# Optimization experiments

Hardware: AMD Instinct MI355X
Metric: run time of the kernel (lower is better)

## Reference

```python
import jax, jax.numpy as jnp
import numpy as np

N = 40000      # nodes
E = 640000     # edges (before self-loops)
F_IN = 32      # num_node_features
H = 8          # n_heads
C = 16         # hidden_channels
G = 1000       # graphs in batch
M = 256        # MLP_neurons
NEG_SLOPE = 0.2


def setup_inputs() -> dict:
    key = jax.random.key(0)
    ks = jax.random.split(key, 24)
    d = {}
    d["x"] = jax.random.normal(ks[0], (N, F_IN), jnp.float32)
    d["edge_index"] = jax.random.randint(ks[1], (2, E), 0, N, dtype=jnp.int32)
    d["batch"] = jnp.sort(jax.random.randint(ks[2], (N,), 0, G, dtype=jnp.int32))
    dims = [F_IN, H * C, H * C]
    k = 3
    for i in range(3):
        fin = dims[i]
        s = 1.0 / np.sqrt(fin)
        d[f"W{i}"] = jax.random.normal(ks[k], (fin, H * C), jnp.float32) * s; k += 1
        d[f"b{i}"] = jnp.zeros((H * C,), jnp.float32)
        d[f"as{i}"] = jax.random.normal(ks[k], (H, C), jnp.float32) * (1.0 / np.sqrt(C)); k += 1
        d[f"ad{i}"] = jax.random.normal(ks[k], (H, C), jnp.float32) * (1.0 / np.sqrt(C)); k += 1
    d["fW0"] = jax.random.normal(ks[k], (H * C, M), jnp.float32) * (1.0 / np.sqrt(H * C)); k += 1
    d["fb0"] = jnp.zeros((M,), jnp.float32)
    d["fW1"] = jax.random.normal(ks[k], (M, M), jnp.float32) * (1.0 / np.sqrt(M)); k += 1
    d["fb1"] = jnp.zeros((M,), jnp.float32)
    d["oW"] = jax.random.normal(ks[k], (M, 2), jnp.float32) * (1.0 / np.sqrt(M)); k += 1
    d["ob"] = jnp.zeros((2,), jnp.float32)
    return d


def _gat_layer(x, W, b, a_src, a_dst, src, dst):
    # x: [N, Fin] -> h: [N, H, C]
    h = (x @ W).reshape(N, H, C)
    al_src = jnp.einsum('nhc,hc->nh', h, a_src)   # [N, H]
    al_dst = jnp.einsum('nhc,hc->nh', h, a_dst)   # [N, H]
    # edge-wise attention logits (gather), LeakyReLU
    e = jax.nn.leaky_relu(al_src[src] + al_dst[dst], NEG_SLOPE)  # [E', H]
    # softmax over incoming edges of each dst node
    emax = jax.ops.segment_max(e, dst, num_segments=N)           # [N, H]
    ex = jnp.exp(e - emax[dst])
    denom = jax.ops.segment_sum(ex, dst, num_segments=N)         # [N, H]
    alpha = ex / denom[dst]
    # weighted scatter-aggregation of source features
    out = jax.ops.segment_sum(alpha[:, :, None] * h[src], dst, num_segments=N)  # [N, H, C]
    return out.reshape(N, H * C) + b


def reference(x, edge_index, batch, W0, b0, as0, ad0, W1, b1, as1, ad1,
              W2, b2, as2, ad2, fW0, fb0, fW1, fb1, oW, ob):
    # PyG GATConv adds self-loops by default
    loops = jnp.arange(N, dtype=edge_index.dtype)
    src = jnp.concatenate([edge_index[0], loops])
    dst = jnp.concatenate([edge_index[1], loops])
    h = x
    for (W, b, a_s, a_d) in ((W0, b0, as0, ad0), (W1, b1, as1, ad1), (W2, b2, as2, ad2)):
        h = jax.nn.relu(_gat_layer(h, W, b, a_s, a_d, src, dst))
    # global mean pool per graph
    sums = jax.ops.segment_sum(h, batch, num_segments=G)                    # [G, H*C]
    cnts = jax.ops.segment_sum(jnp.ones((N,), h.dtype), batch, num_segments=G)
    g = sums / jnp.maximum(cnts, 1.0)[:, None]
    # MLP head (dropout is identity in eval mode)
    g = jax.nn.relu(g @ fW0 + fb0)
    g = jax.nn.relu(g @ fW1 + fb1)
    return g @ oW + ob
```

## Files before the change

### kernel.cpp

```cpp
#include <hip/hip_runtime.h>
#include <hip/hip_fp16.h>
#include <math.h>

#define NN 40000
#define EE 640000
#define EP 680000
#define FIN0 32
#define HC 128
#define GG 1000
#define MM 256
#define SCAN_BLOCKS ((NN + 255) / 256)


__global__ void hist_kernel(const int* __restrict__ ei, int* __restrict__ deg,
                            int* __restrict__ rank) {
    int idx = blockIdx.x * 256 + threadIdx.x;
    if (idx >= EP) return;
    int d = (idx < EE) ? ei[EE + idx] : (idx - EE);
    rank[idx] = atomicAdd(&deg[d], 1);
}

__global__ __launch_bounds__(256) void scan_partial(const int* __restrict__ deg,
                                                    int* __restrict__ part) {
    int b = blockIdx.x, t = threadIdx.x;
    int i = b * 256 + t;
    int v = (i < NN) ? deg[i] : 0;
#pragma unroll
    for (int d = 1; d < 64; d <<= 1) v += __shfl_xor(v, d);
    __shared__ int ws[4];
    if ((t & 63) == 0) ws[t >> 6] = v;
    __syncthreads();
    if (t == 0) part[b] = ws[0] + ws[1] + ws[2] + ws[3];
}

__global__ __launch_bounds__(256) void scan_final(const int* __restrict__ deg,
                                                  const int* __restrict__ part,
                                                  int* __restrict__ offs) {
    int b = blockIdx.x, t = threadIdx.x;
    __shared__ int sbase;
    if (t < 64) {
        int s = 0;
        for (int l = t; l < b; l += 64) s += part[l];
#pragma unroll
        for (int d = 1; d < 64; d <<= 1) s += __shfl_xor(s, d);
        if (t == 0) sbase = s;
    }
    int i = b * 256 + t;
    int v = (i < NN) ? deg[i] : 0;
    __shared__ int tmp[256];
    tmp[t] = v;
    __syncthreads();
    for (int st = 1; st < 256; st <<= 1) {
        int add = (t >= st) ? tmp[t - st] : 0;
        __syncthreads();
        tmp[t] += add;
        __syncthreads();
    }
    int excl = tmp[t] - v + sbase;
    if (i < NN) offs[i] = excl;
    if (i == NN - 1) offs[NN] = excl + v;
}

__global__ void scatter_kernel(const int* __restrict__ ei, const int* __restrict__ offs,
                               const int* __restrict__ rank, int* __restrict__ esrc) {
    int idx = blockIdx.x * 256 + threadIdx.x;
    if (idx >= EP) return;
    int s, d;
    if (idx < EE) { s = ei[idx]; d = ei[EE + idx]; } else { s = idx - EE; d = s; }
    esrc[offs[d] + rank[idx]] = s;
}


template <int FIN>
__global__ __launch_bounds__(256) void proj_kernel(const float* __restrict__ X,
                                                   const float* __restrict__ W,
                                                   const float* __restrict__ a_src,
                                                   const float* __restrict__ a_dst,
                                                   __half* __restrict__ H2,
                                                   float* __restrict__ als,
                                                   float* __restrict__ ald) {
    constexpr int KT = 32;
    static_assert(FIN % KT == 0, "FIN % KT");
    __shared__ float xs[KT][68];
    __shared__ float ws[KT][128];
    int t = threadIdx.x;
    int node0 = blockIdx.x * 64;
    int nt = t & 15;
    int ct = t >> 4;
    float acc[4][8];
#pragma unroll
    for (int i = 0; i < 4; i++)
#pragma unroll
        for (int j = 0; j < 8; j++) acc[i][j] = 0.f;

    for (int kk = 0; kk < FIN; kk += KT) {
#pragma unroll
        for (int r = 0; r < (64 * KT) / 256; r++) {
            int idx = r * 256 + t;
            int n = idx / KT, k = idx % KT;
            xs[k][n] = X[(node0 + n) * FIN + kk + k];
        }
#pragma unroll
        for (int r = 0; r < (KT * 128) / 256; r++) {
            int idx = r * 256 + t;
            int k = idx >> 7, c = idx & 127;
            ws[k][c] = W[(kk + k) * 128 + c];
        }
        __syncthreads();
#pragma unroll
        for (int k = 0; k < KT; k++) {
            const float4 xv = *(const float4*)(&xs[k][4 * nt]);
            const float4 wa = *(const float4*)(&ws[k][8 * ct]);
            const float4 wb = *(const float4*)(&ws[k][8 * ct + 4]);
            float xr[4] = {xv.x, xv.y, xv.z, xv.w};
            float wr[8] = {wa.x, wa.y, wa.z, wa.w, wb.x, wb.y, wb.z, wb.w};
#pragma unroll
            for (int i = 0; i < 4; i++)
#pragma unroll
                for (int j = 0; j < 8; j++) acc[i][j] = fmaf(xr[i], wr[j], acc[i][j]);
        }
        __syncthreads();
    }
#pragma unroll
    for (int i = 0; i < 4; i++) {
        int n = node0 + 4 * nt + i;
        __half2 p0 = __floats2half2_rn(acc[i][0], acc[i][1]);
        __half2 p1 = __floats2half2_rn(acc[i][2], acc[i][3]);
        __half2 p2 = __floats2half2_rn(acc[i][4], acc[i][5]);
        __half2 p3 = __floats2half2_rn(acc[i][6], acc[i][7]);
        uint4 pk;
        pk.x = *(unsigned*)&p0; pk.y = *(unsigned*)&p1;
        pk.z = *(unsigned*)&p2; pk.w = *(unsigned*)&p3;
        *(uint4*)(&H2[(size_t)n * HC + 8 * ct]) = pk;
    }
    float sa[4] = {0.f, 0.f, 0.f, 0.f}, da[4] = {0.f, 0.f, 0.f, 0.f};
#pragma unroll
    for (int j = 0; j < 8; j++) {
        float av = a_src[ct * 8 + j];
        float dv = a_dst[ct * 8 + j];
#pragma unroll
        for (int i = 0; i < 4; i++) {
            sa[i] = fmaf(acc[i][j], av, sa[i]);
            da[i] = fmaf(acc[i][j], dv, da[i]);
        }
    }
#pragma unroll
    for (int i = 0; i < 4; i++) {
        sa[i] += __shfl_xor(sa[i], 16);
        da[i] += __shfl_xor(da[i], 16);
    }
    if ((ct & 1) == 0) {
        int head = ct >> 1;
#pragma unroll
        for (int i = 0; i < 4; i++) {
            int n = node0 + 4 * nt + i;
            als[n * 8 + head] = sa[i];
            ald[n * 8 + head] = da[i];
        }
    }
}


__global__ __launch_bounds__(256) void agg_kernel(const __half* __restrict__ H2,
                                                  const float* __restrict__ als,
                                                  const float* __restrict__ ald,
                                                  const int* __restrict__ offs,
                                                  const int* __restrict__ esrc,
                                                  const float* __restrict__ bias,
                                                  float* __restrict__ OUT) {
    int t = threadIdx.x;
    int n = blockIdx.x * 4 + (t >> 6);
    int t6 = t & 63;
    int c8 = t6 & 15;
    int slot = (t6 >> 4) & 3;
    int hd = c8 >> 1;
    int beg = offs[n], end = offs[n + 1];
    float ad = ald[n * 8 + hd];
    float acc[8] = {0.f, 0.f, 0.f, 0.f, 0.f, 0.f, 0.f, 0.f};
    float denom = 0.f;
    const float4* H4 = (const float4*)H2;

    int p = beg + slot;
    int s_cur = 0; float al_cur = 0.f;
    if (p < end) {
        s_cur = esrc[p];
        al_cur = als[s_cur * 8 + hd];
    }
#pragma unroll 2
    while (p < end) {
        int pn = p + 4;
        int s_nxt = 0;
        if (pn < end) s_nxt = esrc[pn];
        float x = al_cur + ad;
        x = (x > 0.f) ? x : 0.2f * x;
        float w = __expf(x);
        float4 r = H4[(size_t)s_cur * 16 + c8];
        float al_nxt = 0.f;
        if (pn < end) al_nxt = als[s_nxt * 8 + hd];
        __half2 h0 = *(__half2*)&r.x;
        __half2 h1 = *(__half2*)&r.y;
        __half2 h2 = *(__half2*)&r.z;
        __half2 h3 = *(__half2*)&r.w;
        float2 f0 = __half22float2(h0);
        float2 f1 = __half22float2(h1);
        float2 f2 = __half22float2(h2);
        float2 f3 = __half22float2(h3);
        acc[0] = fmaf(w, f0.x, acc[0]); acc[1] = fmaf(w, f0.y, acc[1]);
        acc[2] = fmaf(w, f1.x, acc[2]); acc[3] = fmaf(w, f1.y, acc[3]);
        acc[4] = fmaf(w, f2.x, acc[4]); acc[5] = fmaf(w, f2.y, acc[5]);
        acc[6] = fmaf(w, f3.x, acc[6]); acc[7] = fmaf(w, f3.y, acc[7]);
        denom += w;
        s_cur = s_nxt; al_cur = al_nxt;
        p = pn;
    }
#pragma unroll
    for (int j = 0; j < 8; j++) {
        acc[j] += __shfl_xor(acc[j], 16);
        acc[j] += __shfl_xor(acc[j], 32);
    }
    denom += __shfl_xor(denom, 16);
    denom += __shfl_xor(denom, 32);
    if (slot == 0 && t6 < 16) {
        float inv = 1.0f / denom;
        const float4 ba = ((const float4*)bias)[2 * c8];
        const float4 bb = ((const float4*)bias)[2 * c8 + 1];
        float4 o0, o1;
        o0.x = fmaxf(fmaf(acc[0], inv, ba.x), 0.f);
        o0.y = fmaxf(fmaf(acc[1], inv, ba.y), 0.f);
        o0.z = fmaxf(fmaf(acc[2], inv, ba.z), 0.f);
        o0.w = fmaxf(fmaf(acc[3], inv, ba.w), 0.f);
        o1.x = fmaxf(fmaf(acc[4], inv, bb.x), 0.f);
        o1.y = fmaxf(fmaf(acc[5], inv, bb.y), 0.f);
        o1.z = fmaxf(fmaf(acc[6], inv, bb.z), 0.f);
        o1.w = fmaxf(fmaf(acc[7], inv, bb.w), 0.f);
        ((float4*)OUT)[(size_t)n * 32 + 2 * c8]     = o0;
        ((float4*)OUT)[(size_t)n * 32 + 2 * c8 + 1] = o1;
    }
}


__global__ __launch_bounds__(256) void mlp_fused(const float* __restrict__ B,
                                                 const int* __restrict__ batch,
                                                 const float* __restrict__ fW0,
                                                 const float* __restrict__ fb0,
                                                 const float* __restrict__ fW1,
                                                 const float* __restrict__ fb1,
                                                 const float* __restrict__ oW,
                                                 const float* __restrict__ ob,
                                                 float* __restrict__ out) {
    __shared__ int lo[3];
    __shared__ float rows[2][128];
    __shared__ float g1s[2][256];
    __shared__ float g2s[2][256];
    int t = threadIdx.x;
    int g0 = blockIdx.x * 2;
    if (t < 3) {
        int target = g0 + t;
        int a = 0, b = NN;
        while (a < b) { int mid = (a + b) >> 1; if (batch[mid] < target) a = mid + 1; else b = mid; }
        lo[t] = a;
    }
    __syncthreads();
    {
        int j = t >> 7, c = t & 127;
        int s0 = lo[j], s1 = lo[j + 1];
        float s = 0.f;
        float p0 = 0.f, p1 = 0.f, p2 = 0.f, p3 = 0.f;
        int n = s0;
        for (; n + 3 < s1; n += 4) {
            p0 += B[(size_t)n * 128 + c];
            p1 += B[(size_t)(n + 1) * 128 + c];
            p2 += B[(size_t)(n + 2) * 128 + c];
            p3 += B[(size_t)(n + 3) * 128 + c];
        }
        for (; n < s1; n++) s += B[(size_t)n * 128 + c];
        s += (p0 + p1) + (p2 + p3);
        rows[j][c] = s / fmaxf((float)(s1 - s0), 1.0f);
    }
    __syncthreads();
    float a0 = 0.f, a1 = 0.f;
#pragma unroll 8
    for (int k = 0; k < 128; k++) {
        float w = fW0[k * 256 + t];
        a0 = fmaf(rows[0][k], w, a0);
        a1 = fmaf(rows[1][k], w, a1);
    }
    float b0v = fb0[t];
    g1s[0][t] = fmaxf(a0 + b0v, 0.f);
    g1s[1][t] = fmaxf(a1 + b0v, 0.f);
    __syncthreads();
    a0 = 0.f; a1 = 0.f;
#pragma unroll 8
    for (int k = 0; k < 256; k++) {
        float w = fW1[k * 256 + t];
        a0 = fmaf(g1s[0][k], w, a0);
        a1 = fmaf(g1s[1][k], w, a1);
    }
    float b1v = fb1[t];
    g2s[0][t] = fmaxf(a0 + b1v, 0.f);
    g2s[1][t] = fmaxf(a1 + b1v, 0.f);
    __syncthreads();
    if (t < 64) {
        int jj = t >> 5, l = t & 31;
        float p0 = 0.f, p1 = 0.f;
#pragma unroll
        for (int k = l; k < 256; k += 32) {
            float v = g2s[jj][k];
            p0 = fmaf(v, oW[k * 2 + 0], p0);
            p1 = fmaf(v, oW[k * 2 + 1], p1);
        }
#pragma unroll
        for (int d = 1; d < 32; d <<= 1) {
            p0 += __shfl_xor(p0, d);
            p1 += __shfl_xor(p1, d);
        }
        if (l == 0) {
            out[(g0 + jj) * 2 + 0] = p0 + ob[0];
            out[(g0 + jj) * 2 + 1] = p1 + ob[1];
        }
    }
}


extern "C" void kernel_launch(void* const* d_in, const int* in_sizes, int n_in,
                              void* d_out, int out_size, void* d_ws, size_t ws_size,
                              hipStream_t stream) {
    const float* x    = (const float*)d_in[0];
    const int* ei     = (const int*)d_in[1];
    const int* batch  = (const int*)d_in[2];
    const float* W[3]   = {(const float*)d_in[3], (const float*)d_in[7],  (const float*)d_in[11]};
    const float* bs[3]  = {(const float*)d_in[4], (const float*)d_in[8],  (const float*)d_in[12]};
    const float* asr[3] = {(const float*)d_in[5], (const float*)d_in[9],  (const float*)d_in[13]};
    const float* adt[3] = {(const float*)d_in[6], (const float*)d_in[10], (const float*)d_in[14]};
    const float* fW0 = (const float*)d_in[15];
    const float* fb0 = (const float*)d_in[16];
    const float* fW1 = (const float*)d_in[17];
    const float* fb1 = (const float*)d_in[18];
    const float* oW  = (const float*)d_in[19];
    const float* ob  = (const float*)d_in[20];
    float* out = (float*)d_out;

    char* base = (char*)d_ws;
    size_t off = 0;
    auto alloc = [&](size_t bytes) -> void* {
        void* p = base + off;
        off += (bytes + 255) & ~(size_t)255;
        return p;
    };
    int* deg    = (int*)alloc((size_t)NN * 4);
    int* offs   = (int*)alloc((size_t)(NN + 1) * 4);
    int* part   = (int*)alloc((size_t)SCAN_BLOCKS * 4);
    int* rank   = (int*)alloc((size_t)EP * 4);
    int* esrc   = (int*)alloc((size_t)EP * 4);
    __half* H2  = (__half*)alloc((size_t)NN * HC * 2);
    float* B    = (float*)alloc((size_t)NN * HC * 4);
    float* als  = (float*)alloc((size_t)NN * 8 * 4);
    float* ald  = (float*)alloc((size_t)NN * 8 * 4);

    hipMemsetAsync(deg, 0, (size_t)NN * 4, stream);

    hist_kernel<<<(EP + 255) / 256, 256, 0, stream>>>(ei, deg, rank);
    scan_partial<<<SCAN_BLOCKS, 256, 0, stream>>>(deg, part);
    scan_final<<<SCAN_BLOCKS, 256, 0, stream>>>(deg, part, offs);
    scatter_kernel<<<(EP + 255) / 256, 256, 0, stream>>>(ei, offs, rank, esrc);

    const float* cur = x;
    for (int l = 0; l < 3; l++) {
        if (l == 0) proj_kernel<FIN0><<<NN / 64, 256, 0, stream>>>(cur, W[l], asr[l], adt[l], H2, als, ald);
        else        proj_kernel<HC><<<NN / 64, 256, 0, stream>>>(cur, W[l], asr[l], adt[l], H2, als, ald);
        agg_kernel<<<NN / 4, 256, 0, stream>>>(H2, als, ald, offs, esrc, bs[l], B);
        cur = B;
    }
    mlp_fused<<<GG / 2, 256, 0, stream>>>(B, batch, fW0, fb0, fW1, fb1, oW, ob, out);
}
```

Measured before the change: 319.6 us.

## Enlarge projection tile to 128 nodes, vectorize loads, merge scan kernels

The projection GEMM now computes 128 nodes per block, with an 8x8 register tile per thread instead of 4x8, and loads X and W with float4 accesses. Bounds guards handle the partial last tile. The two-pass prefix scan becomes a single kernel in which each block directly sums all preceding degrees, removing one launch at the cost of redundant reads. The larger register tile raises register pressure, and with only 313 blocks occupancy may drop.

```diff
diff --git a/kernel.cpp b/kernel.cpp
--- a/kernel.cpp
+++ b/kernel.cpp
@@ -10,6 +10,7 @@
 #define GG 1000
 #define MM 256
 #define SCAN_BLOCKS ((NN + 255) / 256)
+#define PROJ_BLOCKS ((NN + 127) / 128)
 
 
 __global__ void hist_kernel(const int* __restrict__ ei, int* __restrict__ deg,
@@ -20,31 +21,19 @@
     rank[idx] = atomicAdd(&deg[d], 1);
 }
 
-__global__ __launch_bounds__(256) void scan_partial(const int* __restrict__ deg,
-                                                    int* __restrict__ part) {
+
+__global__ __launch_bounds__(256) void scan_kernel(const int* __restrict__ deg,
+                                                   int* __restrict__ offs) {
     int b = blockIdx.x, t = threadIdx.x;
-    int i = b * 256 + t;
-    int v = (i < NN) ? deg[i] : 0;
-#pragma unroll
-    for (int d = 1; d < 64; d <<= 1) v += __shfl_xor(v, d);
-    __shared__ int ws[4];
-    if ((t & 63) == 0) ws[t >> 6] = v;
-    __syncthreads();
-    if (t == 0) part[b] = ws[0] + ws[1] + ws[2] + ws[3];
-}
-
-__global__ __launch_bounds__(256) void scan_final(const int* __restrict__ deg,
-                                                  const int* __restrict__ part,
-                                                  int* __restrict__ offs) {
-    int b = blockIdx.x, t = threadIdx.x;
-    __shared__ int sbase;
-    if (t < 64) {
-        int s = 0;
-        for (int l = t; l < b; l += 64) s += part[l];
-#pragma unroll
-        for (int d = 1; d < 64; d <<= 1) s += __shfl_xor(s, d);
-        if (t == 0) sbase = s;
-    }
+    int s = 0;
+    for (int i = t; i < b * 256; i += 256) s += deg[i];
+#pragma unroll
+    for (int d = 1; d < 64; d <<= 1) s += __shfl_xor(s, d);
+    __shared__ int wsum[4];
+    if ((t & 63) == 0) wsum[t >> 6] = s;
+    __syncthreads();
+    int base = wsum[0] + wsum[1] + wsum[2] + wsum[3];
+
     int i = b * 256 + t;
     int v = (i < NN) ? deg[i] : 0;
     __shared__ int tmp[256];
@@ -56,7 +45,7 @@
         tmp[t] += add;
         __syncthreads();
     }
-    int excl = tmp[t] - v + sbase;
+    int excl = tmp[t] - v + base;
     if (i < NN) offs[i] = excl;
     if (i == NN - 1) offs[NN] = excl + v;
 }
@@ -81,81 +70,96 @@
                                                    float* __restrict__ ald) {
     constexpr int KT = 32;
     static_assert(FIN % KT == 0, "FIN % KT");
-    __shared__ float xs[KT][68];
+    __shared__ float xs[KT][132];
     __shared__ float ws[KT][128];
     int t = threadIdx.x;
-    int node0 = blockIdx.x * 64;
+    int node0 = blockIdx.x * 128;
     int nt = t & 15;
     int ct = t >> 4;
-    float acc[4][8];
-#pragma unroll
-    for (int i = 0; i < 4; i++)
+    float acc[8][8];
+#pragma unroll
+    for (int i = 0; i < 8; i++)
 #pragma unroll
         for (int j = 0; j < 8; j++) acc[i][j] = 0.f;
 
     for (int kk = 0; kk < FIN; kk += KT) {
 #pragma unroll
-        for (int r = 0; r < (64 * KT) / 256; r++) {
+        for (int r = 0; r < 4; r++) {
             int idx = r * 256 + t;
-            int n = idx / KT, k = idx % KT;
-            xs[k][n] = X[(node0 + n) * FIN + kk + k];
-        }
-#pragma unroll
-        for (int r = 0; r < (KT * 128) / 256; r++) {
+            int n = idx >> 3;
+            int k = (idx & 7) * 4;
+            int gn = node0 + n;
+            if (gn >= NN) gn = NN - 1;
+            float4 v = *(const float4*)(&X[(size_t)gn * FIN + kk + k]);
+            xs[k + 0][n] = v.x;
+            xs[k + 1][n] = v.y;
+            xs[k + 2][n] = v.z;
+            xs[k + 3][n] = v.w;
+        }
+#pragma unroll
+        for (int r = 0; r < 4; r++) {
             int idx = r * 256 + t;
-            int k = idx >> 7, c = idx & 127;
-            ws[k][c] = W[(kk + k) * 128 + c];
+            int k = idx >> 5;
+            int c = (idx & 31) * 4;
+            *(float4*)(&ws[k][c]) = *(const float4*)(&W[(size_t)(kk + k) * 128 + c]);
         }
         __syncthreads();
 #pragma unroll
         for (int k = 0; k < KT; k++) {
-            const float4 xv = *(const float4*)(&xs[k][4 * nt]);
+            const float4 xa = *(const float4*)(&xs[k][8 * nt]);
+            const float4 xb = *(const float4*)(&xs[k][8 * nt + 4]);
             const float4 wa = *(const float4*)(&ws[k][8 * ct]);
             const float4 wb = *(const float4*)(&ws[k][8 * ct + 4]);
-            float xr[4] = {xv.x, xv.y, xv.z, xv.w};
+            float xr[8] = {xa.x, xa.y, xa.z, xa.w, xb.x, xb.y, xb.z, xb.w};
             float wr[8] = {wa.x, wa.y, wa.z, wa.w, wb.x, wb.y, wb.z, wb.w};
 #pragma unroll
-            for (int i = 0; i < 4; i++)
+            for (int i = 0; i < 8; i++)
 #pragma unroll
                 for (int j = 0; j < 8; j++) acc[i][j] = fmaf(xr[i], wr[j], acc[i][j]);
         }
         __syncthreads();
     }
 #pragma unroll
-    for (int i = 0; i < 4; i++) {
-        int n = node0 + 4 * nt + i;
-        __half2 p0 = __floats2half2_rn(acc[i][0], acc[i][1]);
-        __half2 p1 = __floats2half2_rn(acc[i][2], acc[i][3]);
-        __half2 p2 = __floats2half2_rn(acc[i][4], acc[i][5]);
-        __half2 p3 = __floats2half2_rn(acc[i][6], acc[i][7]);
-        uint4 pk;
-        pk.x = *(unsigned*)&p0; pk.y = *(unsigned*)&p1;
-        pk.z = *(unsigned*)&p2; pk.w = *(unsigned*)&p3;
-        *(uint4*)(&H2[(size_t)n * HC + 8 * ct]) = pk;
-    }
-    float sa[4] = {0.f, 0.f, 0.f, 0.f}, da[4] = {0.f, 0.f, 0.f, 0.f};
+    for (int i = 0; i < 8; i++) {
+        int n = node0 + 8 * nt + i;
+        if (n < NN) {
+            __half2 p0 = __floats2half2_rn(acc[i][0], acc[i][1]);
+            __half2 p1 = __floats2half2_rn(acc[i][2], acc[i][3]);
+            __half2 p2 = __floats2half2_rn(acc[i][4], acc[i][5]);
+            __half2 p3 = __floats2half2_rn(acc[i][6], acc[i][7]);
+            uint4 pk;
+            pk.x = *(unsigned*)&p0; pk.y = *(unsigned*)&p1;
+            pk.z = *(unsigned*)&p2; pk.w = *(unsigned*)&p3;
+            *(uint4*)(&H2[(size_t)n * HC + 8 * ct]) = pk;
+        }
+    }
+    float sa[8], da[8];
+#pragma unroll
+    for (int i = 0; i < 8; i++) { sa[i] = 0.f; da[i] = 0.f; }
 #pragma unroll
     for (int j = 0; j < 8; j++) {
         float av = a_src[ct * 8 + j];
         float dv = a_dst[ct * 8 + j];
 #pragma unroll
-        for (int i = 0; i < 4; i++) {
+        for (int i = 0; i < 8; i++) {
             sa[i] = fmaf(acc[i][j], av, sa[i]);
             da[i] = fmaf(acc[i][j], dv, da[i]);
         }
     }
 #pragma unroll
-    for (int i = 0; i < 4; i++) {
+    for (int i = 0; i < 8; i++) {
         sa[i] += __shfl_xor(sa[i], 16);
         da[i] += __shfl_xor(da[i], 16);
     }
     if ((ct & 1) == 0) {
         int head = ct >> 1;
 #pragma unroll
-        for (int i = 0; i < 4; i++) {
-            int n = node0 + 4 * nt + i;
-            als[n * 8 + head] = sa[i];
-            ald[n * 8 + head] = da[i];
+        for (int i = 0; i < 8; i++) {
+            int n = node0 + 8 * nt + i;
+            if (n < NN) {
+                als[n * 8 + head] = sa[i];
+                ald[n * 8 + head] = da[i];
+            }
         }
     }
 }
@@ -349,7 +353,6 @@
     };
     int* deg    = (int*)alloc((size_t)NN * 4);
     int* offs   = (int*)alloc((size_t)(NN + 1) * 4);
-    int* part   = (int*)alloc((size_t)SCAN_BLOCKS * 4);
     int* rank   = (int*)alloc((size_t)EP * 4);
     int* esrc   = (int*)alloc((size_t)EP * 4);
     __half* H2  = (__half*)alloc((size_t)NN * HC * 2);
@@ -360,14 +363,13 @@
     hipMemsetAsync(deg, 0, (size_t)NN * 4, stream);
 
     hist_kernel<<<(EP + 255) / 256, 256, 0, stream>>>(ei, deg, rank);
-    scan_partial<<<SCAN_BLOCKS, 256, 0, stream>>>(deg, part);
-    scan_final<<<SCAN_BLOCKS, 256, 0, stream>>>(deg, part, offs);
+    scan_kernel<<<SCAN_BLOCKS, 256, 0, stream>>>(deg, offs);
     scatter_kernel<<<(EP + 255) / 256, 256, 0, stream>>>(ei, offs, rank, esrc);
 
     const float* cur = x;
     for (int l = 0; l < 3; l++) {
-        if (l == 0) proj_kernel<FIN0><<<NN / 64, 256, 0, stream>>>(cur, W[l], asr[l], adt[l], H2, als, ald);
-        else        proj_kernel<HC><<<NN / 64, 256, 0, stream>>>(cur, W[l], asr[l], adt[l], H2, als, ald);
+        if (l == 0) proj_kernel<FIN0><<<PROJ_BLOCKS, 256, 0, stream>>>(cur, W[l], asr[l], adt[l], H2, als, ald);
+        else        proj_kernel<HC><<<PROJ_BLOCKS, 256, 0, stream>>>(cur, W[l], asr[l], adt[l], H2, als, ald);
         agg_kernel<<<NN / 4, 256, 0, stream>>>(H2, als, ald, offs, esrc, bs[l], B);
         cur = B;
     }
```

New measurement: 351.2 us. +9.9%, slower.
